# Kernel tuning notes

Hardware: AMD Instinct MI355X
Metric: run time of the kernel (lower is better)

The kernel has to match this reference:

```python
import jax, jax.numpy as jnp
import numpy as np

B, S, D, H = 4, 2048, 1024, 16
DK = D // H
DFF = 4 * D
EPS = 1e-6


def setup_inputs() -> dict:
    key = jax.random.key(0)
    ks = jax.random.split(key, 16)
    s = 0.02
    return {
        "x": jax.random.normal(ks[0], (B, S, D), jnp.float32),
        "mask": jax.random.randint(ks[1], (B, 1, 1, S), 0, 2, jnp.int32),
        "wq": jax.random.normal(ks[2], (D, D), jnp.float32) * s,
        "bq": jnp.zeros((D,), jnp.float32),
        "wk": jax.random.normal(ks[3], (D, D), jnp.float32) * s,
        "bk": jnp.zeros((D,), jnp.float32),
        "wv": jax.random.normal(ks[4], (D, D), jnp.float32) * s,
        "bv": jnp.zeros((D,), jnp.float32),
        "wo": jax.random.normal(ks[5], (D, D), jnp.float32) * s,
        "bo": jnp.zeros((D,), jnp.float32),
        "w1": jax.random.normal(ks[6], (DFF, D), jnp.float32) * s,
        "b1": jnp.zeros((DFF,), jnp.float32),
        "w2": jax.random.normal(ks[7], (D, DFF), jnp.float32) * s,
        "b2": jnp.zeros((D,), jnp.float32),
        "a1": jnp.ones((1,), jnp.float32),
        "c1": jnp.zeros((1,), jnp.float32),
        "a2": jnp.ones((1,), jnp.float32),
        "c2": jnp.zeros((1,), jnp.float32),
    }


def _layernorm(x, alpha, bias):
    # source: alpha * (x - mean) / (std + eps) + bias, torch std is unbiased
    mean = jnp.mean(x, axis=-1, keepdims=True)
    std = jnp.std(x, axis=-1, keepdims=True, ddof=1)
    return alpha * (x - mean) / (std + EPS) + bias


def _mha(x, mask, wq, bq, wk, bk, wv, bv, wo, bo):
    q = (x @ wq.T + bq).reshape(B, S, H, DK).transpose(0, 2, 1, 3)  # [B,H,S,DK]
    k = (x @ wk.T + bk).reshape(B, S, H, DK).transpose(0, 2, 1, 3)
    v = (x @ wv.T + bv).reshape(B, S, H, DK).transpose(0, 2, 1, 3)
    scores = jnp.einsum("bhqd,bhkd->bhqk", q, k) / jnp.sqrt(jnp.float32(DK))
    scores = jnp.where(mask == 0, jnp.float32(-1e9), scores)
    attn = jax.nn.softmax(scores, axis=-1)
    out = jnp.einsum("bhqk,bhkd->bhqd", attn, v)  # [B,H,S,DK]
    out = out.transpose(0, 2, 1, 3).reshape(B, S, D)
    return out @ wo.T + bo


def reference(x, mask, wq, bq, wk, bk, wv, bv, wo, bo, w1, b1, w2, b2, a1, c1, a2, c2):
    # residual 1: x + MHA(LN(x))  (dropout = identity in eval)
    h = x + _mha(_layernorm(x, a1, c1), mask, wq, bq, wk, bk, wv, bv, wo, bo)
    # residual 2: h + FFN(LN(h))
    hn = _layernorm(h, a2, c2)
    ffn = jax.nn.relu(hn @ w1.T + b1) @ w2.T + b2
    return h + ffn
```

## Files before the change

### kernel.cpp

```cpp
#include <hip/hip_runtime.h>
#include <math.h>

static constexpr int B  = 4;
static constexpr int S  = 2048;
static constexpr int D  = 1024;
static constexpr int H  = 16;
static constexpr int DFF = 4096;

typedef __attribute__((ext_vector_type(8))) short short8;
typedef __attribute__((ext_vector_type(8))) unsigned short ushort8;
typedef __attribute__((ext_vector_type(4))) unsigned short ushort4v;
typedef __attribute__((ext_vector_type(4))) float f32x4;

__device__ __forceinline__ float b2f(unsigned short u) {
  unsigned int x = ((unsigned int)u) << 16;
  float f;
  __builtin_memcpy(&f, &x, 4);
  return f;
}
__device__ __forceinline__ unsigned short f2b(float f) {
  unsigned int x;
  __builtin_memcpy(&x, &f, 4);
  x += 0x7fffu + ((x >> 16) & 1u);
  return (unsigned short)(x >> 16);
}

__device__ __forceinline__ f32x4 mfma16(short8 a, short8 b, f32x4 c) {
  return __builtin_amdgcn_mfma_f32_16x16x32_bf16(a, b, c, 0, 0, 0);
}

__device__ __forceinline__ void gload_lds16(const void* gsrc, void* ldst) {
  __builtin_amdgcn_global_load_lds(
      (__attribute__((address_space(1))) void*)(uintptr_t)gsrc,
      (__attribute__((address_space(3))) void*)ldst, 16, 0, 0);
}

__global__ __launch_bounds__(256) void convert_k(const float* __restrict__ s,
                                                 unsigned short* __restrict__ d, int n) {
  const int i = (blockIdx.x * 256 + threadIdx.x) * 4;
  if (i < n) {
    f32x4 v = *(const f32x4*)(s + i);
    ushort4v o;
#pragma unroll
    for (int j = 0; j < 4; j++) o[j] = f2b(v[j]);
    *(ushort4v*)(d + i) = o;
  }
}

__global__ __launch_bounds__(256) void ln_fused(const float* __restrict__ x,
                                                const float* __restrict__ ap,
                                                const float* __restrict__ cp,
                                                unsigned short* __restrict__ out) {
  const int row = blockIdx.x, tid = threadIdx.x;
  const size_t base = (size_t)row * D;
  float v[4];
  float s = 0.f, sq = 0.f;
#pragma unroll
  for (int i = 0; i < 4; i++) {
    v[i] = x[base + tid + i * 256];
    s += v[i];
    sq += v[i] * v[i];
  }
#pragma unroll
  for (int o = 32; o > 0; o >>= 1) {
    s += __shfl_xor(s, o);
    sq += __shfl_xor(sq, o);
  }
  __shared__ __align__(16) float rs[4], rq[4];
  const int wave = tid >> 6, lane = tid & 63;
  if (lane == 0) {
    rs[wave] = s;
    rq[wave] = sq;
  }
  __syncthreads();
  const float S1 = rs[0] + rs[1] + rs[2] + rs[3];
  const float S2 = rq[0] + rq[1] + rq[2] + rq[3];
  const float mean = S1 * (1.f / 1024.f);
  const float var = fmaxf(0.f, (S2 - 1024.f * mean * mean) * (1.f / 1023.f));
  const float rstd = 1.f / (sqrtf(var) + 1e-6f);
  const float alpha = ap[0], beta = cp[0];
#pragma unroll
  for (int i = 0; i < 4; i++)
    out[base + tid + i * 256] = f2b(alpha * (v[i] - mean) * rstd + beta);
}

template <int EPI>
__global__ __launch_bounds__(256) void gemm_bb(
    const unsigned short* __restrict__ A, const unsigned short* __restrict__ W,
    const float* __restrict__ bias0, const float* __restrict__ bias1,
    const float* __restrict__ bias2, const float* __restrict__ resid,
    void* __restrict__ out, unsigned short* __restrict__ outK,
    unsigned short* __restrict__ outV, int M, int N, int K, int ldw) {
  __shared__ __align__(16) unsigned short As[128 * 32];
  __shared__ __align__(16) unsigned short Bs[128 * 32];
  const int tid = threadIdx.x;
  const int lane = tid & 63, wave = tid >> 6;
  const int quad = lane >> 4, l16 = lane & 15;
  const int m0 = blockIdx.y * 128, n0 = blockIdx.x * 128;
  const int wm = (wave >> 1) * 64, wn = (wave & 1) * 64;

  f32x4 acc[4][4];
#pragma unroll
  for (int i = 0; i < 4; i++)
#pragma unroll
    for (int j = 0; j < 4; j++) acc[i][j] = {0.f, 0.f, 0.f, 0.f};

  const int rA = tid >> 2;
  const int kc = (tid & 3) * 8;

  for (int k0 = 0; k0 < K; k0 += 32) {
    __syncthreads();
#pragma unroll
    for (int i = 0; i < 2; i++) {
      const int row = i * 64 + rA;
      gload_lds16(&A[(size_t)(m0 + row) * K + k0 + kc], &As[(i * 256 + wave * 64) * 8]);
      gload_lds16(&W[(size_t)(n0 + row) * ldw + k0 + kc], &Bs[(i * 256 + wave * 64) * 8]);
    }
    __syncthreads();
    short8 af[4], bf[4];
#pragma unroll
    for (int t = 0; t < 4; t++) {
      af[t] = *(const short8*)&As[(wm + t * 16 + l16) * 32 + quad * 8];
      bf[t] = *(const short8*)&Bs[(wn + t * 16 + l16) * 32 + quad * 8];
    }
#pragma unroll
    for (int mt = 0; mt < 4; mt++)
#pragma unroll
      for (int nt = 0; nt < 4; nt++) acc[mt][nt] = mfma16(af[mt], bf[nt], acc[mt][nt]);
  }

  if (EPI == 4) {
    const int band = (n0 + wn) >> 10;
    const float* bp = band == 0 ? bias0 : (band == 1 ? bias1 : bias2);
#pragma unroll
    for (int nt = 0; nt < 4; nt++) {
      const int col = n0 + wn + nt * 16 + l16;
      const int cl = col & 1023;
      const float bv = bp[cl];
#pragma unroll
      for (int mt = 0; mt < 4; mt++) {
#pragma unroll
        for (int r = 0; r < 4; r++) {
          const int row = m0 + wm + mt * 16 + quad * 4 + r;
          const float v = acc[mt][nt][r] + bv;
          if (band == 0)
            ((unsigned short*)out)[(size_t)row * 1024 + cl] = f2b(v);
          else if (band == 1)
            outK[(size_t)row * 1024 + cl] = f2b(v);
          else
            outV[((size_t)((row >> 11) * 1024 + cl)) * 2048 + (row & 2047)] = f2b(v);
        }
      }
    }
  } else {
#pragma unroll
    for (int nt = 0; nt < 4; nt++) {
      const int col = n0 + wn + nt * 16 + l16;
      const float bv = (EPI == 3) ? 0.f : bias0[col];
#pragma unroll
      for (int mt = 0; mt < 4; mt++) {
#pragma unroll
        for (int r = 0; r < 4; r++) {
          const int row = m0 + wm + mt * 16 + quad * 4 + r;
          const size_t idx = (size_t)row * N + col;
          float v = acc[mt][nt][r] + bv;
          if (EPI == 2) {
            v = fmaxf(v, 0.f);
            ((unsigned short*)out)[idx] = f2b(v);
          } else {
            v += resid[idx];
            ((float*)out)[idx] = v;
          }
        }
      }
    }
  }
}

__global__ __launch_bounds__(256) void attn_kernel(unsigned short* __restrict__ Q,
                                                   const unsigned short* __restrict__ Kb,
                                                   const unsigned short* __restrict__ VT,
                                                   const int* __restrict__ mask) {
  constexpr int PAD = 72;
  __shared__ __align__(16) unsigned short Ks[64 * PAD];
  __shared__ __align__(16) unsigned short VTs[64 * PAD];
  __shared__ __align__(16) unsigned short Pb[4][16 * PAD];

  const int tid = threadIdx.x, lane = tid & 63, wave = tid >> 6;
  const int quad = lane >> 4, l16 = lane & 15;
  const int q0 = blockIdx.x * 64;
  const int b = blockIdx.y >> 4, h = blockIdx.y & 15;

  short8 qf0, qf1;
  {
    const int qr = q0 + wave * 16 + l16;
    const unsigned short* qp = &Q[((size_t)(b * S) + qr) * D + h * 64 + quad * 8];
    qf0 = *(const short8*)qp;
    qf1 = *(const short8*)(qp + 32);
  }

  float l_r[4] = {0.f, 0.f, 0.f, 0.f};
  f32x4 o_acc[4];
#pragma unroll
  for (int t = 0; t < 4; t++) o_acc[t] = {0.f, 0.f, 0.f, 0.f};

  const int rT = tid >> 3;
  const int cT = (tid & 7) * 8;

  for (int kt = 0; kt < S / 64; kt++) {
    const int k0 = kt * 64;
    ushort8 kv[2], vv[2];
#pragma unroll
    for (int i = 0; i < 2; i++) {
      const int r = i * 32 + rT;
      kv[i] = *(const ushort8*)&Kb[((size_t)(b * S) + k0 + r) * D + h * 64 + cT];
      vv[i] = *(const ushort8*)&VT[((size_t)(blockIdx.y * 64 + r)) * S + k0 + cT];
    }
    __syncthreads();
#pragma unroll
    for (int i = 0; i < 2; i++) {
      const int r = i * 32 + rT;
      *(ushort8*)&Ks[r * PAD + cT] = kv[i];
      *(ushort8*)&VTs[r * PAD + cT] = vv[i];
    }
    __syncthreads();

    f32x4 sc[4];
#pragma unroll
    for (int nt = 0; nt < 4; nt++) sc[nt] = {0.f, 0.f, 0.f, 0.f};
#pragma unroll
    for (int nt = 0; nt < 4; nt++) {
      short8 kf0 = *(const short8*)&Ks[(nt * 16 + l16) * PAD + quad * 8];
      short8 kf1 = *(const short8*)&Ks[(nt * 16 + l16) * PAD + 32 + quad * 8];
      sc[nt] = mfma16(qf0, kf0, sc[nt]);
      sc[nt] = mfma16(qf1, kf1, sc[nt]);
    }

#pragma unroll
    for (int nt = 0; nt < 4; nt++) {
      const float madd = mask[b * S + k0 + nt * 16 + l16] ? -12.f : -42.f;
#pragma unroll
      for (int r = 0; r < 4; r++) {
        const float p = __expf(fmaf(sc[nt][r], 0.125f, madd));
        l_r[r] += p;
        Pb[wave][(quad * 4 + r) * PAD + nt * 16 + l16] = f2b(p);
      }
    }

    short8 pf0 = *(const short8*)&Pb[wave][l16 * PAD + quad * 8];
    short8 pf1 = *(const short8*)&Pb[wave][l16 * PAD + 32 + quad * 8];
#pragma unroll
    for (int nt = 0; nt < 4; nt++) {
      short8 vf0 = *(const short8*)&VTs[(nt * 16 + l16) * PAD + quad * 8];
      short8 vf1 = *(const short8*)&VTs[(nt * 16 + l16) * PAD + 32 + quad * 8];
      o_acc[nt] = mfma16(pf0, vf0, o_acc[nt]);
      o_acc[nt] = mfma16(pf1, vf1, o_acc[nt]);
    }
  }

#pragma unroll
  for (int o = 1; o < 16; o <<= 1) {
#pragma unroll
    for (int r = 0; r < 4; r++) l_r[r] += __shfl_xor(l_r[r], o);
  }

#pragma unroll
  for (int r = 0; r < 4; r++) {
    const float inv = 1.f / l_r[r];
    const int q = q0 + wave * 16 + quad * 4 + r;
#pragma unroll
    for (int nt = 0; nt < 4; nt++) {
      const int dk = nt * 16 + l16;
      Q[((size_t)(b * S) + q) * D + h * 64 + dk] = f2b(o_acc[nt][r] * inv);
    }
  }
}

__global__ __launch_bounds__(256) void stats_kernel(const float* __restrict__ x,
                                                    float2* __restrict__ st) {
  const int row = blockIdx.x, tid = threadIdx.x;
  const size_t base = (size_t)row * D;
  float s = 0.f, sq = 0.f;
#pragma unroll
  for (int i = 0; i < 4; i++) {
    const float v = x[base + tid + i * 256];
    s += v;
    sq += v * v;
  }
#pragma unroll
  for (int o = 32; o > 0; o >>= 1) {
    s += __shfl_xor(s, o);
    sq += __shfl_xor(sq, o);
  }
  __shared__ __align__(16) float rs[4], rq[4];
  const int wave = tid >> 6, lane = tid & 63;
  if (lane == 0) {
    rs[wave] = s;
    rq[wave] = sq;
  }
  __syncthreads();
  if (tid == 0) {
    const float S1 = rs[0] + rs[1] + rs[2] + rs[3];
    const float S2 = rq[0] + rq[1] + rq[2] + rq[3];
    const float mean = S1 * (1.f / 1024.f);
    const float var = fmaxf(0.f, (S2 - 1024.f * mean * mean) * (1.f / 1023.f));
    const float rstd = 1.f / (sqrtf(var) + 1e-6f);
    st[row] = make_float2(mean, rstd);
  }
}

template <int EPI, int NORM, int AF32, int OUTF32>
__global__ __launch_bounds__(256) void gemm_bt(
    const void* __restrict__ Ap, const float* __restrict__ W,
    const float* __restrict__ bias, const float* __restrict__ resid,
    void* __restrict__ outp, const float2* __restrict__ stats,
    const float* __restrict__ alpha_p, const float* __restrict__ beta_p,
    int M, int N, int K, int ldw) {
  __shared__ __align__(16) unsigned short As[128 * 32];
  __shared__ __align__(16) unsigned short Bs[128 * 32];
  const int tid = threadIdx.x;
  const int lane = tid & 63, wave = tid >> 6;
  const int quad = lane >> 4, l16 = lane & 15;
  const int m0 = blockIdx.y * 128, n0 = blockIdx.x * 128;
  const int wm = (wave >> 1) * 64, wn = (wave & 1) * 64;

  float alpha = 0.f, beta = 0.f;
  if (NORM) {
    alpha = alpha_p[0];
    beta = beta_p[0];
  }

  f32x4 acc[4][4];
#pragma unroll
  for (int i = 0; i < 4; i++)
#pragma unroll
    for (int j = 0; j < 4; j++) acc[i][j] = {0.f, 0.f, 0.f, 0.f};

  const int rA = tid >> 2;
  const int kc = (tid & 3) * 8;

  for (int k0 = 0; k0 < K; k0 += 32) {
    ushort8 av[2], bv8[2];
#pragma unroll
    for (int i = 0; i < 2; i++) {
      const int row = i * 64 + rA;
      if (AF32) {
        const float* ap = (const float*)Ap + (size_t)(m0 + row) * K + k0 + kc;
        f32x4 a0 = *(const f32x4*)ap;
        f32x4 a1 = *(const f32x4*)(ap + 4);
        if (NORM) {
          const float2 st = stats[m0 + row];
#pragma unroll
          for (int j = 0; j < 4; j++) {
            a0[j] = alpha * (a0[j] - st.x) * st.y + beta;
            a1[j] = alpha * (a1[j] - st.x) * st.y + beta;
          }
        }
#pragma unroll
        for (int j = 0; j < 4; j++) {
          av[i][j] = f2b(a0[j]);
          av[i][j + 4] = f2b(a1[j]);
        }
      } else {
        av[i] = *(const ushort8*)((const unsigned short*)Ap +
                                  (size_t)(m0 + row) * K + k0 + kc);
      }
      const float* wp = W + (size_t)(n0 + row) * ldw + k0 + kc;
      f32x4 w0 = *(const f32x4*)wp;
      f32x4 w1 = *(const f32x4*)(wp + 4);
#pragma unroll
      for (int j = 0; j < 4; j++) {
        bv8[i][j] = f2b(w0[j]);
        bv8[i][j + 4] = f2b(w1[j]);
      }
    }
    __syncthreads();
#pragma unroll
    for (int i = 0; i < 2; i++) {
      const int row = i * 64 + rA;
      *(ushort8*)&As[row * 32 + kc] = av[i];
      *(ushort8*)&Bs[row * 32 + kc] = bv8[i];
    }
    __syncthreads();
    short8 af[4], bf[4];
#pragma unroll
    for (int t = 0; t < 4; t++) {
      af[t] = *(const short8*)&As[(wm + t * 16 + l16) * 32 + quad * 8];
      bf[t] = *(const short8*)&Bs[(wn + t * 16 + l16) * 32 + quad * 8];
    }
#pragma unroll
    for (int mt = 0; mt < 4; mt++)
#pragma unroll
      for (int nt = 0; nt < 4; nt++) acc[mt][nt] = mfma16(af[mt], bf[nt], acc[mt][nt]);
  }

#pragma unroll
  for (int nt = 0; nt < 4; nt++) {
    const int col = n0 + wn + nt * 16 + l16;
    const float bv = (EPI == 3) ? 0.f : bias[col];
#pragma unroll
    for (int mt = 0; mt < 4; mt++) {
#pragma unroll
      for (int r = 0; r < 4; r++) {
        const int row = m0 + wm + mt * 16 + quad * 4 + r;
        float v = acc[mt][nt][r] + bv;
        if (EPI == 2) v = fmaxf(v, 0.f);
        if (EPI == 4) {
          const size_t vtidx =
              ((size_t)((row >> 11) * 1024 + col)) * 2048 + (row & 2047);
          ((unsigned short*)outp)[vtidx] = f2b(v);
        } else {
          const size_t idx = (size_t)row * N + col;
          if (EPI == 1 || EPI == 3) v += resid[idx];
          if (OUTF32)
            ((float*)outp)[idx] = v;
          else
            ((unsigned short*)outp)[idx] = f2b(v);
        }
      }
    }
  }
}

extern "C" void kernel_launch(void* const* d_in, const int* in_sizes, int n_in,
                              void* d_out, int out_size, void* d_ws, size_t ws_size,
                              hipStream_t stream) {
  (void)in_sizes; (void)n_in; (void)out_size;
  const float* x  = (const float*)d_in[0];
  const int* mask = (const int*)d_in[1];
  const float* wq = (const float*)d_in[2];
  const float* bq = (const float*)d_in[3];
  const float* wk = (const float*)d_in[4];
  const float* bk = (const float*)d_in[5];
  const float* wv = (const float*)d_in[6];
  const float* bv = (const float*)d_in[7];
  const float* wo = (const float*)d_in[8];
  const float* bo = (const float*)d_in[9];
  const float* w1 = (const float*)d_in[10];
  const float* b1 = (const float*)d_in[11];
  const float* w2 = (const float*)d_in[12];
  const float* b2 = (const float*)d_in[13];
  const float* a1 = (const float*)d_in[14];
  const float* c1 = (const float*)d_in[15];
  const float* a2 = (const float*)d_in[16];
  const float* c2 = (const float*)d_in[17];

  char* ws = (char*)d_ws;
  const size_t MB = 1 << 20;
  const int M = B * S;
  dim3 blk(256);
  dim3 gAttn(S / 64, B * H);

  if (ws_size >= 89 * MB) {
    const int tier2 = (ws_size >= 121 * MB);
    unsigned short* wqkv_b = (unsigned short*)(ws + 0);
    unsigned short* wo_b   = (unsigned short*)(ws + 6 * MB);
    unsigned short* w1_b   = (unsigned short*)(ws + 8 * MB);
    unsigned short* w2_b   = (unsigned short*)(ws + 16 * MB);
    unsigned short* ln1x   = (unsigned short*)(ws + 25 * MB);
    unsigned short* q      = (unsigned short*)(ws + 41 * MB);
    unsigned short* kk     = (unsigned short*)(ws + 57 * MB);
    unsigned short* vt     = (unsigned short*)(ws + 73 * MB);
    float*          hbuf   = (float*)(ws + 57 * MB);
    unsigned short* ln2x   = (unsigned short*)(ws + 25 * MB);
    unsigned short* ffn1q  = (unsigned short*)(ws + 41 * MB);
    unsigned short* ffn1h  = (unsigned short*)(ws + 89 * MB);
    float* outb = (float*)d_out;

    convert_k<<<1024, blk, 0, stream>>>(wq, wqkv_b, 1048576);
    convert_k<<<1024, blk, 0, stream>>>(wk, wqkv_b + 1048576, 1048576);
    convert_k<<<1024, blk, 0, stream>>>(wv, wqkv_b + 2097152, 1048576);
    convert_k<<<1024, blk, 0, stream>>>(wo, wo_b, 1048576);
    convert_k<<<4096, blk, 0, stream>>>(w1, w1_b, 4194304);
    convert_k<<<4096, blk, 0, stream>>>(w2, w2_b, 4194304);

    ln_fused<<<M, blk, 0, stream>>>(x, a1, c1, ln1x);
    gemm_bb<4><<<dim3(24, 64), blk, 0, stream>>>(ln1x, wqkv_b, bq, bk, bv, nullptr,
                                                 q, kk, vt, M, 3072, D, D);
    attn_kernel<<<gAttn, blk, 0, stream>>>(q, kk, vt, mask);
    gemm_bb<1><<<dim3(8, 64), blk, 0, stream>>>(q, wo_b, bo, nullptr, nullptr, x,
                                                hbuf, nullptr, nullptr, M, D, D, D);
    ln_fused<<<M, blk, 0, stream>>>(hbuf, a2, c2, ln2x);

    if (tier2) {
      gemm_bb<2><<<dim3(16, 64), blk, 0, stream>>>(ln2x, w1_b, b1, nullptr, nullptr,
                                                   nullptr, ffn1h, nullptr, nullptr,
                                                   M, 2048, D, D);
      gemm_bb<1><<<dim3(8, 64), blk, 0, stream>>>(ffn1h, w2_b, b2, nullptr, nullptr,
                                                  hbuf, outb, nullptr, nullptr,
                                                  M, D, 2048, DFF);
      gemm_bb<2><<<dim3(16, 64), blk, 0, stream>>>(ln2x, w1_b + (size_t)2048 * D,
                                                   b1 + 2048, nullptr, nullptr, nullptr,
                                                   ffn1h, nullptr, nullptr, M, 2048, D, D);
      gemm_bb<3><<<dim3(8, 64), blk, 0, stream>>>(ffn1h, w2_b + 2048, nullptr, nullptr,
                                                  nullptr, outb, outb, nullptr, nullptr,
                                                  M, D, 2048, DFF);
    } else {
      for (int i = 0; i < 4; i++) {
        gemm_bb<2><<<dim3(8, 64), blk, 0, stream>>>(ln2x, w1_b + (size_t)i * 1024 * D,
                                                    b1 + i * 1024, nullptr, nullptr,
                                                    nullptr, ffn1q, nullptr, nullptr,
                                                    M, 1024, D, D);
        if (i == 0)
          gemm_bb<1><<<dim3(8, 64), blk, 0, stream>>>(ffn1q, w2_b + i * 1024, b2, nullptr,
                                                      nullptr, hbuf, outb, nullptr, nullptr,
                                                      M, D, 1024, DFF);
        else
          gemm_bb<3><<<dim3(8, 64), blk, 0, stream>>>(ffn1q, w2_b + i * 1024, nullptr,
                                                      nullptr, nullptr, outb, outb, nullptr,
                                                      nullptr, M, D, 1024, DFF);
      }
    }
  } else {
    float2* stats1 = (float2*)(ws + 0);
    float2* stats2 = (float2*)(ws + 128 * 1024);
    unsigned short* q    = (unsigned short*)(ws + 1 * MB);
    unsigned short* kk   = (unsigned short*)(ws + 17 * MB);
    unsigned short* vt   = (unsigned short*)(ws + 33 * MB);
    float*          hbuf = (float*)(ws + 17 * MB);
    unsigned short* ffn1 = (unsigned short*)(ws + 1 * MB);
    float* outb = (float*)d_out;
    dim3 gD(D / 128, M / 128);

    stats_kernel<<<M, blk, 0, stream>>>(x, stats1);
    gemm_bt<0, 1, 1, 0><<<gD, blk, 0, stream>>>(x, wq, bq, nullptr, q, stats1, a1, c1, M, D, D, D);
    gemm_bt<0, 1, 1, 0><<<gD, blk, 0, stream>>>(x, wk, bk, nullptr, kk, stats1, a1, c1, M, D, D, D);
    gemm_bt<4, 1, 1, 0><<<gD, blk, 0, stream>>>(x, wv, bv, nullptr, vt, stats1, a1, c1, M, D, D, D);
    attn_kernel<<<gAttn, blk, 0, stream>>>(q, kk, vt, mask);
    gemm_bt<1, 0, 0, 1><<<gD, blk, 0, stream>>>(q, wo, bo, x, hbuf, nullptr, nullptr, nullptr, M, D, D, D);
    stats_kernel<<<M, blk, 0, stream>>>(hbuf, stats2);
    for (int i = 0; i < 4; i++) {
      gemm_bt<2, 1, 1, 0><<<gD, blk, 0, stream>>>(hbuf, w1 + (size_t)i * 1024 * D,
                                                  b1 + i * 1024, nullptr, ffn1, stats2,
                                                  a2, c2, M, 1024, D, D);
      if (i == 0)
        gemm_bt<1, 0, 0, 1><<<gD, blk, 0, stream>>>(ffn1, w2 + i * 1024, b2, hbuf, outb,
                                                    nullptr, nullptr, nullptr, M, D, 1024, DFF);
      else
        gemm_bt<3, 0, 0, 1><<<gD, blk, 0, stream>>>(ffn1, w2 + i * 1024, nullptr, outb, outb,
                                                    nullptr, nullptr, nullptr, M, D, 1024, DFF);
    }
  }
}
```

Before: 663.7 us.

## Batch weight conversions, transpose attention score MFMA, run full-width FFN when workspace allows

Merges six weight-conversion launches into one 2D-grid kernel. In attention, swaps the MFMA operands so each lane holds four consecutive keys for one query. That allows a vector mask load, a packed P store and a single scalar row-sum reduced with two shuffles. When the workspace is at least 152 MB, the FFN runs as one full-DFF GEMM pair instead of two halves, which costs a larger intermediate buffer.

After: 652.8 us. Within noise of the previous version (-1.6%).

```diff
diff --git a/kernel.cpp b/kernel.cpp
--- a/kernel.cpp
+++ b/kernel.cpp
@@ -35,15 +35,20 @@
       (__attribute__((address_space(3))) void*)ldst, 16, 0, 0);
 }
 
-__global__ __launch_bounds__(256) void convert_k(const float* __restrict__ s,
-                                                 unsigned short* __restrict__ d, int n) {
+struct CvtArgs {
+  const float* s[6];
+  unsigned short* d[6];
+  int n[6];
+};
+__global__ __launch_bounds__(256) void convert6(CvtArgs a) {
+  const int seg = blockIdx.y;
   const int i = (blockIdx.x * 256 + threadIdx.x) * 4;
-  if (i < n) {
-    f32x4 v = *(const f32x4*)(s + i);
+  if (i < a.n[seg]) {
+    f32x4 v = *(const f32x4*)(a.s[seg] + i);
     ushort4v o;
 #pragma unroll
     for (int j = 0; j < 4; j++) o[j] = f2b(v[j]);
-    *(ushort4v*)(d + i) = o;
+    *(ushort4v*)(a.d[seg] + i) = o;
   }
 }
 
@@ -199,7 +204,7 @@
     qf1 = *(const short8*)(qp + 32);
   }
 
-  float l_r[4] = {0.f, 0.f, 0.f, 0.f};
+  float l_acc = 0.f;
   f32x4 o_acc[4];
 #pragma unroll
   for (int t = 0; t < 4; t++) o_acc[t] = {0.f, 0.f, 0.f, 0.f};
@@ -232,19 +237,26 @@
     for (int nt = 0; nt < 4; nt++) {
       short8 kf0 = *(const short8*)&Ks[(nt * 16 + l16) * PAD + quad * 8];
       short8 kf1 = *(const short8*)&Ks[(nt * 16 + l16) * PAD + 32 + quad * 8];
-      sc[nt] = mfma16(qf0, kf0, sc[nt]);
-      sc[nt] = mfma16(qf1, kf1, sc[nt]);
+      sc[nt] = mfma16(kf0, qf0, sc[nt]);
+      sc[nt] = mfma16(kf1, qf1, sc[nt]);
     }
 
 #pragma unroll
     for (int nt = 0; nt < 4; nt++) {
-      const float madd = mask[b * S + k0 + nt * 16 + l16] ? -12.f : -42.f;
-#pragma unroll
-      for (int r = 0; r < 4; r++) {
-        const float p = __expf(fmaf(sc[nt][r], 0.125f, madd));
-        l_r[r] += p;
-        Pb[wave][(quad * 4 + r) * PAD + nt * 16 + l16] = f2b(p);
-      }
+      const int4 mv = *(const int4*)&mask[b * S + k0 + nt * 16 + quad * 4];
+      ushort4v pk;
+      {
+        const float p0 = __expf(fmaf(sc[nt][0], 0.125f, mv.x ? -12.f : -42.f));
+        const float p1 = __expf(fmaf(sc[nt][1], 0.125f, mv.y ? -12.f : -42.f));
+        const float p2 = __expf(fmaf(sc[nt][2], 0.125f, mv.z ? -12.f : -42.f));
+        const float p3 = __expf(fmaf(sc[nt][3], 0.125f, mv.w ? -12.f : -42.f));
+        l_acc += p0 + p1 + p2 + p3;
+        pk[0] = f2b(p0);
+        pk[1] = f2b(p1);
+        pk[2] = f2b(p2);
+        pk[3] = f2b(p3);
+      }
+      *(ushort4v*)&Pb[wave][l16 * PAD + nt * 16 + quad * 4] = pk;
     }
 
     short8 pf0 = *(const short8*)&Pb[wave][l16 * PAD + quad * 8];
@@ -258,15 +270,13 @@
     }
   }
 
-#pragma unroll
-  for (int o = 1; o < 16; o <<= 1) {
-#pragma unroll
-    for (int r = 0; r < 4; r++) l_r[r] += __shfl_xor(l_r[r], o);
-  }
+  l_acc += __shfl_xor(l_acc, 16);
+  l_acc += __shfl_xor(l_acc, 32);
 
 #pragma unroll
   for (int r = 0; r < 4; r++) {
-    const float inv = 1.f / l_r[r];
+    const float lr = __shfl(l_acc, quad * 4 + r);
+    const float inv = 1.f / lr;
     const int q = q0 + wave * 16 + quad * 4 + r;
 #pragma unroll
     for (int nt = 0; nt < 4; nt++) {
@@ -452,6 +462,7 @@
   dim3 gAttn(S / 64, B * H);
 
   if (ws_size >= 89 * MB) {
+    const int tier3 = (ws_size >= 152 * MB);
     const int tier2 = (ws_size >= 121 * MB);
     unsigned short* wqkv_b = (unsigned short*)(ws + 0);
     unsigned short* wo_b   = (unsigned short*)(ws + 6 * MB);
@@ -465,14 +476,17 @@
     unsigned short* ln2x   = (unsigned short*)(ws + 25 * MB);
     unsigned short* ffn1q  = (unsigned short*)(ws + 41 * MB);
     unsigned short* ffn1h  = (unsigned short*)(ws + 89 * MB);
+    unsigned short* ffn1f  = (unsigned short*)(ws + 89 * MB);
     float* outb = (float*)d_out;
 
-    convert_k<<<1024, blk, 0, stream>>>(wq, wqkv_b, 1048576);
-    convert_k<<<1024, blk, 0, stream>>>(wk, wqkv_b + 1048576, 1048576);
-    convert_k<<<1024, blk, 0, stream>>>(wv, wqkv_b + 2097152, 1048576);
-    convert_k<<<1024, blk, 0, stream>>>(wo, wo_b, 1048576);
-    convert_k<<<4096, blk, 0, stream>>>(w1, w1_b, 4194304);
-    convert_k<<<4096, blk, 0, stream>>>(w2, w2_b, 4194304);
+    CvtArgs ca;
+    ca.s[0] = wq; ca.d[0] = wqkv_b;            ca.n[0] = 1048576;
+    ca.s[1] = wk; ca.d[1] = wqkv_b + 1048576;  ca.n[1] = 1048576;
+    ca.s[2] = wv; ca.d[2] = wqkv_b + 2097152;  ca.n[2] = 1048576;
+    ca.s[3] = wo; ca.d[3] = wo_b;              ca.n[3] = 1048576;
+    ca.s[4] = w1; ca.d[4] = w1_b;              ca.n[4] = 4194304;
+    ca.s[5] = w2; ca.d[5] = w2_b;              ca.n[5] = 4194304;
+    convert6<<<dim3(4096, 6), blk, 0, stream>>>(ca);
 
     ln_fused<<<M, blk, 0, stream>>>(x, a1, c1, ln1x);
     gemm_bb<4><<<dim3(24, 64), blk, 0, stream>>>(ln1x, wqkv_b, bq, bk, bv, nullptr,
@@ -482,7 +496,14 @@
                                                 hbuf, nullptr, nullptr, M, D, D, D);
     ln_fused<<<M, blk, 0, stream>>>(hbuf, a2, c2, ln2x);
 
-    if (tier2) {
+    if (tier3) {
+      gemm_bb<2><<<dim3(32, 64), blk, 0, stream>>>(ln2x, w1_b, b1, nullptr, nullptr,
+                                                   nullptr, ffn1f, nullptr, nullptr,
+                                                   M, DFF, D, D);
+      gemm_bb<1><<<dim3(8, 64), blk, 0, stream>>>(ffn1f, w2_b, b2, nullptr, nullptr,
+                                                  hbuf, outb, nullptr, nullptr,
+                                                  M, D, DFF, DFF);
+    } else if (tier2) {
       gemm_bb<2><<<dim3(16, 64), blk, 0, stream>>>(ln2x, w1_b, b1, nullptr, nullptr,
                                                    nullptr, ffn1h, nullptr, nullptr,
                                                    M, 2048, D, D);
```
